# Kernel optimization log

Hardware: AMD Instinct MI355X
Metric: run time of the kernel (lower is better)

Reference implementation:

```python
import jax, jax.numpy as jnp
import numpy as np

ALPHA = 1.702   # swiglu_alpha
LIMIT = 7.0     # swiglu_limit
EPS = 1e-5      # norm_eps
E = 16          # num_experts
K = 4           # experts_per_token


def _swiglu(h):
    # interleaved split as in torch: even cols -> glu, odd cols -> linear
    x_glu = jnp.minimum(h[..., ::2], LIMIT)
    # faithful to source bug: clamp(min=limit, max=limit) == constant limit
    x_lin = jnp.clip(h[..., 1::2], LIMIT, LIMIT)
    return x_glu * jax.nn.sigmoid(ALPHA * x_glu) * (x_lin + 1.0)


def setup_inputs() -> dict:
    key = jax.random.key(0)
    ks = jax.random.split(key, 7)
    B, T, H, I = 1, 2048, 1024, 1024
    x = jax.random.normal(ks[0], (B, T, H), jnp.float32)
    scale = jnp.ones((H,), jnp.float32)
    gate_w = jax.random.normal(ks[1], (E, H), jnp.float32) * 0.02
    gate_b = jnp.zeros((E,), jnp.float32)
    mlp1_w = jax.random.normal(ks[2], (E, 2 * I, H), jnp.float32) * 0.02
    mlp1_b = jax.random.normal(ks[3], (E, 2 * I), jnp.float32) * 0.02
    mlp2_w = jax.random.normal(ks[4], (E, H, I), jnp.float32) * 0.02
    mlp2_b = jax.random.normal(ks[5], (E, H), jnp.float32) * 0.02
    return dict(x=x, scale=scale, gate_w=gate_w, gate_b=gate_b,
                mlp1_w=mlp1_w, mlp1_b=mlp1_b, mlp2_w=mlp2_w, mlp2_b=mlp2_b)


def reference(x, scale, gate_w, gate_b, mlp1_w, mlp1_b, mlp2_w, mlp2_b):
    # RMSNorm (fp32 math, identity cast here since inputs are fp32)
    t = x * jax.lax.rsqrt(jnp.mean(x * x, axis=-1, keepdims=True) + EPS) * scale
    # gate + top-k routing (sorted descending, matching torch.topk sorted=True)
    g = jnp.einsum('bth,eh->bte', t, gate_w) + gate_b          # [B,T,E]
    vals, idx = jax.lax.top_k(g, K)                            # [B,T,K]
    w = jax.nn.softmax(vals, axis=-1)                          # [B,T,K]
    # route[b,t,e] = sum_k w[b,t,k] * [idx[b,t,k]==e]  (top-k indices distinct)
    route = jnp.sum(jax.nn.one_hot(idx, E, dtype=t.dtype) * w[..., None], axis=-2)
    route_e = jnp.moveaxis(route, -1, 0)                       # [E,B,T]
    # grouped dense-per-expert computation instead of per-token weight gather:
    # mathematically identical output, avoids materializing [B,T,K,2I,H] gathers
    def step(acc, p):
        w1, b1, w2, b2, r = p
        h = jnp.einsum('bth,ih->bti', t, w1) + b1              # [B,T,2I]
        s = _swiglu(h)                                         # [B,T,I]
        y = jnp.einsum('bti,hi->bth', s, w2) + b2              # [B,T,H]
        return acc + r[..., None] * y, None
    acc, _ = jax.lax.scan(step, jnp.zeros_like(x),
                          (mlp1_w, mlp1_b, mlp2_w, mlp2_b, route_e))
    return x + acc
```

## Files before the change

kernel.cpp:

```cpp
#include <hip/hip_runtime.h>
#include <hip/hip_bf16.h>

typedef __bf16 bf16;
typedef __bf16 bf16x4 __attribute__((ext_vector_type(4)));
typedef __bf16 bf16x8 __attribute__((ext_vector_type(8)));
typedef float f32x4 __attribute__((ext_vector_type(4)));

constexpr int TKN  = 2048;
constexpr int HD   = 1024;
constexpr int NEXP = 16;
constexpr int KSEL = 4;
constexpr int IDIM = 1024;
constexpr int I2   = 2048;
constexpr int NROW = TKN * KSEL;

__device__ __forceinline__ void async_copy16(const void* g, void* l) {
  __builtin_amdgcn_global_load_lds((__attribute__((address_space(1))) void*)g,
                                   (__attribute__((address_space(3))) void*)l,
                                   16, 0, 0);
}

__global__ __launch_bounds__(256) void k_norm_gate(
    const float* __restrict__ x, const float* __restrict__ scale,
    const float* __restrict__ gate_w, const float* __restrict__ gate_b,
    float* __restrict__ out, bf16* __restrict__ tN,
    int* __restrict__ eids, float* __restrict__ wts)
{
  __shared__ float tLds[HD];
  __shared__ float red[4];
  __shared__ float gsh[NEXP];
  const int tid = threadIdx.x;
  const int tok = blockIdx.x;
  const int wid = tid >> 6, lane = tid & 63;

  const float4 x4 = *(const float4*)(x + (size_t)tok * HD + tid * 4);
  float ss = x4.x * x4.x + x4.y * x4.y + x4.z * x4.z + x4.w * x4.w;
  #pragma unroll
  for (int off = 32; off > 0; off >>= 1) ss += __shfl_down(ss, off);
  if (lane == 0) red[wid] = ss;
  __syncthreads();
  ss = red[0] + red[1] + red[2] + red[3];
  const float r = rsqrtf(ss * (1.0f / HD) + 1e-5f);

  const float4 s4 = *(const float4*)(scale + tid * 4);
  float4 t4;
  t4.x = x4.x * r * s4.x; t4.y = x4.y * r * s4.y;
  t4.z = x4.z * r * s4.z; t4.w = x4.w * r * s4.w;
  *(float4*)(out + (size_t)tok * HD + tid * 4) = x4;
  tLds[tid * 4 + 0] = t4.x; tLds[tid * 4 + 1] = t4.y;
  tLds[tid * 4 + 2] = t4.z; tLds[tid * 4 + 3] = t4.w;
  bf16x4 tb;
  tb[0] = (bf16)t4.x; tb[1] = (bf16)t4.y; tb[2] = (bf16)t4.z; tb[3] = (bf16)t4.w;
  *(bf16x4*)(tN + (size_t)tok * HD + tid * 4) = tb;
  __syncthreads();

  {
    const int e = tid >> 4, l16 = tid & 15;
    float p = 0.f;
    const float* gw = gate_w + (size_t)e * HD;
    for (int j = l16; j < HD; j += 16) p += tLds[j] * gw[j];
    p += __shfl_xor(p, 8); p += __shfl_xor(p, 4);
    p += __shfl_xor(p, 2); p += __shfl_xor(p, 1);
    if (l16 == 0) gsh[e] = p + gate_b[e];
  }
  __syncthreads();

  if (tid == 0) {
    float g[NEXP];
    #pragma unroll
    for (int i = 0; i < NEXP; ++i) g[i] = gsh[i];
    int   bi[KSEL]; float bv[KSEL];
    #pragma unroll
    for (int k = 0; k < KSEL; ++k) {
      float best = -1e30f; int b = 0;
      for (int i = 0; i < NEXP; ++i) if (g[i] > best) { best = g[i]; b = i; }
      bv[k] = best; bi[k] = b; g[b] = -1e30f;
    }
    const float m = bv[0];
    float wv[KSEL], sum = 0.f;
    #pragma unroll
    for (int k = 0; k < KSEL; ++k) { wv[k] = __expf(bv[k] - m); sum += wv[k]; }
    const float inv = 1.0f / sum;
    #pragma unroll
    for (int k = 0; k < KSEL; ++k) {
      eids[tok * KSEL + k] = bi[k];
      wts[tok * KSEL + k]  = wv[k] * inv;
    }
  }
}

__global__ __launch_bounds__(256) void k_route(
    const int* __restrict__ eids, const float* __restrict__ wts,
    int* __restrict__ cntg, int* __restrict__ segg,
    int* __restrict__ rowTok, float* __restrict__ rowW, int* __restrict__ rowOf)
{
  __shared__ int hcnt[NEXP], hoff[NEXP], hrun[NEXP];
  const int tid = threadIdx.x;
  if (tid < NEXP) { hcnt[tid] = 0; hrun[tid] = 0; }
  __syncthreads();
  for (int i = tid; i < NROW; i += 256) atomicAdd(&hcnt[eids[i]], 1);
  __syncthreads();
  if (tid == 0) {
    int s = 0;
    for (int e = 0; e < NEXP; ++e) { hoff[e] = s; segg[e] = s; cntg[e] = hcnt[e]; s += hcnt[e]; }
  }
  __syncthreads();
  for (int i = tid; i < NROW; i += 256) {
    const int e = eids[i];
    const int slot = atomicAdd(&hrun[e], 1);
    const int row = hoff[e] + slot;
    rowTok[row] = i >> 2;
    rowW[row]   = wts[i];
    rowOf[i]    = row;
  }
}

__global__ __launch_bounds__(256) void k_cvt_all(const float* __restrict__ w1,
                                                 const float* __restrict__ w2,
                                                 bf16* __restrict__ w1b,
                                                 bf16* __restrict__ w2b) {
  const size_t bid = blockIdx.x;
  if (bid < 8192) {
    const size_t f = bid * 256 + threadIdx.x;
    const size_t row = f >> 7;
    const int    off = (int)(f & 127) * 8;
    const size_t e = row >> 10, n = row & 1023;
    const float* s = w1 + (e * 2048 + 2 * n) * 1024 + off;
    const float4 a = *(const float4*)(s);
    const float4 b = *(const float4*)(s + 4);
    bf16x8 o;
    o[0] = (bf16)a.x; o[1] = (bf16)a.y; o[2] = (bf16)a.z; o[3] = (bf16)a.w;
    o[4] = (bf16)b.x; o[5] = (bf16)b.y; o[6] = (bf16)b.z; o[7] = (bf16)b.w;
    *(bf16x8*)(w1b + row * 1024 + off) = o;
  } else {
    const size_t f = (bid - 8192) * 256 + threadIdx.x;
    const size_t base = f * 8;
    const float4 a = *(const float4*)(w2 + base);
    const float4 b = *(const float4*)(w2 + base + 4);
    bf16x8 o;
    o[0] = (bf16)a.x; o[1] = (bf16)a.y; o[2] = (bf16)a.z; o[3] = (bf16)a.w;
    o[4] = (bf16)b.x; o[5] = (bf16)b.y; o[6] = (bf16)b.z; o[7] = (bf16)b.w;
    *(bf16x8*)(w2b + base) = o;
  }
}


__global__ __launch_bounds__(256) void k_gemm1v2(
    const bf16* __restrict__ tN, const bf16* __restrict__ w1b,
    const float* __restrict__ b1, const int* __restrict__ cnt,
    const int* __restrict__ segOff, const int* __restrict__ rowTok,
    bf16* __restrict__ sBuf)
{
  const int e = blockIdx.z, mt = blockIdx.y, nt = blockIdx.x;
  const int rows = cnt[e];
  if (mt * 64 >= rows) return;
  const int soff = segOff[e];
  __shared__ __align__(16) bf16 Asm[2 * 64 * 32];
  __shared__ __align__(16) bf16 Bsm[2 * 128 * 32];
  const int tid = threadIdx.x;
  const int wid = tid >> 6, lane = tid & 63;
  const int quad = lane >> 4, l16 = lane & 15;
  const int wm = wid & 1, wn = wid >> 1;

  const int r0 = wid * 16 + (lane >> 2);
  const int colE = (lane & 3) * 8;
  const int mA = min(mt * 64 + r0, rows - 1);
  const char* gA  = (const char*)(tN + (size_t)rowTok[soff + mA] * HD + colE);
  const int n0 = nt * 128;
  const char* gB0 = (const char*)(w1b + ((size_t)e * IDIM + n0 + r0) * HD + colE);
  const char* gB1 = (const char*)(w1b + ((size_t)e * IDIM + n0 + 64 + r0) * HD + colE);
  bf16* lA  = Asm + wid * 512;
  bf16* lB0 = Bsm + wid * 512;
  bf16* lB1 = Bsm + 2048 + wid * 512;

  const f32x4 zero = {0.f, 0.f, 0.f, 0.f};
  f32x4 acc[2][4];
  #pragma unroll
  for (int i = 0; i < 2; ++i)
    #pragma unroll
    for (int j = 0; j < 4; ++j) acc[i][j] = zero;

  for (int kt = 0; kt < 16; ++kt) {
    async_copy16(gA, lA);
    async_copy16(gB0, lB0);
    async_copy16(gB1, lB1);
    async_copy16(gA + 64, lA + 2048);
    async_copy16(gB0 + 64, lB0 + 4096);
    async_copy16(gB1 + 64, lB1 + 4096);
    gA += 128; gB0 += 128; gB1 += 128;
    __syncthreads();
    bf16x8 av[2];
    #pragma unroll
    for (int s = 0; s < 2; ++s) {
      av[0] = *(const bf16x8*)(Asm + s * 2048 + (wm * 32 + 0 * 16 + l16) * 32 + quad * 8);
      av[1] = *(const bf16x8*)(Asm + s * 2048 + (wm * 32 + 1 * 16 + l16) * 32 + quad * 8);
      #pragma unroll
      for (int j = 0; j < 4; ++j) {
        const bf16x8 bv = *(const bf16x8*)(Bsm + s * 4096 + (wn * 64 + j * 16 + l16) * 32 + quad * 8);
        acc[0][j] = __builtin_amdgcn_mfma_f32_16x16x32_bf16(av[0], bv, acc[0][j], 0, 0, 0);
        acc[1][j] = __builtin_amdgcn_mfma_f32_16x16x32_bf16(av[1], bv, acc[1][j], 0, 0, 0);
      }
    }
    __syncthreads();
  }

  const int mbase = mt * 64 + wm * 32;
  #pragma unroll
  for (int j = 0; j < 4; ++j) {
    const int ncol = n0 + wn * 64 + j * 16 + l16;
    const float bias = b1[(size_t)e * I2 + 2 * ncol];
    #pragma unroll
    for (int i = 0; i < 2; ++i) {
      #pragma unroll
      for (int rg = 0; rg < 4; ++rg) {
        const int gm = mbase + i * 16 + quad * 4 + rg;
        if (gm < rows) {
          const float h  = acc[i][j][rg] + bias;
          const float xg = fminf(h, 7.0f);
          const float s  = xg * (1.0f / (1.0f + __expf(-1.702f * xg))) * 8.0f;
          sBuf[((size_t)soff + gm) * IDIM + ncol] = (bf16)s;
        }
      }
    }
  }
}

template <bool USEY>
__global__ __launch_bounds__(256) void k_gemm2v2(
    const bf16* __restrict__ sBuf, const bf16* __restrict__ w2b,
    const float* __restrict__ b2, const int* __restrict__ cnt,
    const int* __restrict__ segOff, const int* __restrict__ rowTok,
    const float* __restrict__ rowW, bf16* __restrict__ yBuf,
    float* __restrict__ out)
{
  const int e = blockIdx.z, mt = blockIdx.y, nt = blockIdx.x;
  const int rows = cnt[e];
  if (mt * 64 >= rows) return;
  const int soff = segOff[e];
  __shared__ __align__(16) bf16 Asm[2 * 64 * 32];
  __shared__ __align__(16) bf16 Bsm[2 * 128 * 32];
  const int tid = threadIdx.x;
  const int wid = tid >> 6, lane = tid & 63;
  const int quad = lane >> 4, l16 = lane & 15;
  const int wm = wid & 1, wn = wid >> 1;

  const int r0 = wid * 16 + (lane >> 2);
  const int colE = (lane & 3) * 8;
  const int mA = min(mt * 64 + r0, rows - 1);
  const char* gA  = (const char*)(sBuf + ((size_t)soff + mA) * IDIM + colE);
  const int n0 = nt * 128;
  const char* gB0 = (const char*)(w2b + ((size_t)e * HD + n0 + r0) * IDIM + colE);
  const char* gB1 = (const char*)(w2b + ((size_t)e * HD + n0 + 64 + r0) * IDIM + colE);
  bf16* lA  = Asm + wid * 512;
  bf16* lB0 = Bsm + wid * 512;
  bf16* lB1 = Bsm + 2048 + wid * 512;

  const f32x4 zero = {0.f, 0.f, 0.f, 0.f};
  f32x4 acc[2][4];
  #pragma unroll
  for (int i = 0; i < 2; ++i)
    #pragma unroll
    for (int j = 0; j < 4; ++j) acc[i][j] = zero;

  for (int kt = 0; kt < 16; ++kt) {
    async_copy16(gA, lA);
    async_copy16(gB0, lB0);
    async_copy16(gB1, lB1);
    async_copy16(gA + 64, lA + 2048);
    async_copy16(gB0 + 64, lB0 + 4096);
    async_copy16(gB1 + 64, lB1 + 4096);
    gA += 128; gB0 += 128; gB1 += 128;
    __syncthreads();
    bf16x8 av[2];
    #pragma unroll
    for (int s = 0; s < 2; ++s) {
      av[0] = *(const bf16x8*)(Asm + s * 2048 + (wm * 32 + 0 * 16 + l16) * 32 + quad * 8);
      av[1] = *(const bf16x8*)(Asm + s * 2048 + (wm * 32 + 1 * 16 + l16) * 32 + quad * 8);
      #pragma unroll
      for (int j = 0; j < 4; ++j) {
        const bf16x8 bv = *(const bf16x8*)(Bsm + s * 4096 + (wn * 64 + j * 16 + l16) * 32 + quad * 8);
        acc[0][j] = __builtin_amdgcn_mfma_f32_16x16x32_bf16(av[0], bv, acc[0][j], 0, 0, 0);
        acc[1][j] = __builtin_amdgcn_mfma_f32_16x16x32_bf16(av[1], bv, acc[1][j], 0, 0, 0);
      }
    }
    __syncthreads();
  }

  const int mbase = mt * 64 + wm * 32;
  #pragma unroll
  for (int j = 0; j < 4; ++j) {
    const int ncol = n0 + wn * 64 + j * 16 + l16;
    const float bias = b2[(size_t)e * HD + ncol];
    #pragma unroll
    for (int i = 0; i < 2; ++i) {
      #pragma unroll
      for (int rg = 0; rg < 4; ++rg) {
        const int gm = mbase + i * 16 + quad * 4 + rg;
        if (gm < rows) {
          if constexpr (USEY) {
            yBuf[((size_t)soff + gm) * HD + ncol] = (bf16)(acc[i][j][rg] + bias);
          } else {
            atomicAdd(out + (size_t)rowTok[soff + gm] * HD + ncol,
                      rowW[soff + gm] * (acc[i][j][rg] + bias));
          }
        }
      }
    }
  }
}

__global__ __launch_bounds__(256) void k_finalize(
    const float* __restrict__ x, const bf16* __restrict__ yBuf,
    const int* __restrict__ rowOf, const float* __restrict__ wts,
    float* __restrict__ out)
{
  const int tok = blockIdx.x;
  const int tid = threadIdx.x;
  const int r0 = rowOf[tok * 4 + 0], r1 = rowOf[tok * 4 + 1];
  const int r2 = rowOf[tok * 4 + 2], r3 = rowOf[tok * 4 + 3];
  const float w0 = wts[tok * 4 + 0], w1 = wts[tok * 4 + 1];
  const float w2 = wts[tok * 4 + 2], w3 = wts[tok * 4 + 3];
  const int col = tid * 4;
  float4 o = *(const float4*)(x + (size_t)tok * HD + col);
  const bf16x4 y0 = *(const bf16x4*)(yBuf + (size_t)r0 * HD + col);
  const bf16x4 y1 = *(const bf16x4*)(yBuf + (size_t)r1 * HD + col);
  const bf16x4 y2 = *(const bf16x4*)(yBuf + (size_t)r2 * HD + col);
  const bf16x4 y3 = *(const bf16x4*)(yBuf + (size_t)r3 * HD + col);
  o.x += w0 * (float)y0[0] + w1 * (float)y1[0] + w2 * (float)y2[0] + w3 * (float)y3[0];
  o.y += w0 * (float)y0[1] + w1 * (float)y1[1] + w2 * (float)y2[1] + w3 * (float)y3[1];
  o.z += w0 * (float)y0[2] + w1 * (float)y1[2] + w2 * (float)y2[2] + w3 * (float)y3[2];
  o.w += w0 * (float)y0[3] + w1 * (float)y1[3] + w2 * (float)y2[3] + w3 * (float)y3[3];
  *(float4*)(out + (size_t)tok * HD + col) = o;
}

__global__ __launch_bounds__(256) void k_gemm1_fb(
    const bf16* __restrict__ tN, const float* __restrict__ w1,
    const float* __restrict__ b1, const int* __restrict__ cnt,
    const int* __restrict__ segOff, const int* __restrict__ rowTok,
    bf16* __restrict__ sBuf)
{
  const int e = blockIdx.z, mt = blockIdx.y, nt = blockIdx.x;
  const int rows = cnt[e];
  if (mt * 128 >= rows) return;
  const int soff = segOff[e];
  __shared__ __align__(16) bf16 Asm[128 * 32];
  __shared__ __align__(16) bf16 Bsm[128 * 32];
  const int tid = threadIdx.x;
  const int wid = tid >> 6, lane = tid & 63;
  const int quad = lane >> 4, l16 = lane & 15;
  const int wm = wid & 1, wn = wid >> 1;
  const int r0 = wid * 16 + (lane >> 2);
  const int r1 = 64 + r0;
  const int colE = (lane & 3) * 8;
  const int m0 = min(mt * 128 + r0, rows - 1);
  const int m1 = min(mt * 128 + r1, rows - 1);
  const char* gA0 = (const char*)(tN + (size_t)rowTok[soff + m0] * HD + colE);
  const char* gA1 = (const char*)(tN + (size_t)rowTok[soff + m1] * HD + colE);
  bf16* lA0 = Asm + wid * 512;
  bf16* lA1 = Asm + 2048 + wid * 512;
  const int brow = tid >> 3;
  const int bkk  = (tid & 7) * 4;
  const int n0 = nt * 128;
  const float* gB = w1 + (size_t)e * I2 * HD + (size_t)(2 * (n0 + brow)) * HD + bkk;

  const f32x4 zero = {0.f, 0.f, 0.f, 0.f};
  f32x4 acc[4][4];
  #pragma unroll
  for (int i = 0; i < 4; ++i)
    #pragma unroll
    for (int j = 0; j < 4; ++j) acc[i][j] = zero;

  for (int kt = 0; kt < 32; ++kt) {
    async_copy16(gA0, lA0);
    async_copy16(gA1, lA1);
    gA0 += 64; gA1 += 64;
    #pragma unroll
    for (int q = 0; q < 4; ++q) {
      const float4 v = *(const float4*)(gB + (size_t)q * 64 * HD);
      bf16x4 c;
      c[0] = (bf16)v.x; c[1] = (bf16)v.y; c[2] = (bf16)v.z; c[3] = (bf16)v.w;
      *(bf16x4*)(Bsm + (q * 32 + brow) * 32 + bkk) = c;
    }
    gB += 32;
    __syncthreads();
    bf16x8 av[4], bv[4];
    #pragma unroll
    for (int i = 0; i < 4; ++i)
      av[i] = *(const bf16x8*)(Asm + (wm * 64 + i * 16 + l16) * 32 + quad * 8);
    #pragma unroll
    for (int j = 0; j < 4; ++j)
      bv[j] = *(const bf16x8*)(Bsm + (wn * 64 + j * 16 + l16) * 32 + quad * 8);
    #pragma unroll
    for (int i = 0; i < 4; ++i)
      #pragma unroll
      for (int j = 0; j < 4; ++j)
        acc[i][j] = __builtin_amdgcn_mfma_f32_16x16x32_bf16(av[i], bv[j], acc[i][j], 0, 0, 0);
    __syncthreads();
  }
  const int mbase = mt * 128 + wm * 64;
  #pragma unroll
  for (int j = 0; j < 4; ++j) {
    const int ncol = n0 + wn * 64 + j * 16 + l16;
    const float bias = b1[(size_t)e * I2 + 2 * ncol];
    #pragma unroll
    for (int i = 0; i < 4; ++i) {
      #pragma unroll
      for (int rg = 0; rg < 4; ++rg) {
        const int gm = mbase + i * 16 + quad * 4 + rg;
        if (gm < rows) {
          const float h  = acc[i][j][rg] + bias;
          const float xg = fminf(h, 7.0f);
          const float s  = xg * (1.0f / (1.0f + __expf(-1.702f * xg))) * 8.0f;
          sBuf[((size_t)soff + gm) * IDIM + ncol] = (bf16)s;
        }
      }
    }
  }
}

__global__ __launch_bounds__(256) void k_gemm2_fb(
    const bf16* __restrict__ sBuf, const float* __restrict__ w2,
    const float* __restrict__ b2, const int* __restrict__ cnt,
    const int* __restrict__ segOff, const int* __restrict__ rowTok,
    const float* __restrict__ rowW, float* __restrict__ out)
{
  const int e = blockIdx.z, mt = blockIdx.y, nt = blockIdx.x;
  const int rows = cnt[e];
  if (mt * 128 >= rows) return;
  const int soff = segOff[e];
  __shared__ __align__(16) bf16 Asm[128 * 32];
  __shared__ __align__(16) bf16 Bsm[128 * 32];
  const int tid = threadIdx.x;
  const int wid = tid >> 6, lane = tid & 63;
  const int quad = lane >> 4, l16 = lane & 15;
  const int wm = wid & 1, wn = wid >> 1;
  const int r0 = wid * 16 + (lane >> 2);
  const int r1 = 64 + r0;
  const int colE = (lane & 3) * 8;
  const int m0 = min(mt * 128 + r0, rows - 1);
  const int m1 = min(mt * 128 + r1, rows - 1);
  const char* gA0 = (const char*)(sBuf + ((size_t)soff + m0) * IDIM + colE);
  const char* gA1 = (const char*)(sBuf + ((size_t)soff + m1) * IDIM + colE);
  bf16* lA0 = Asm + wid * 512;
  bf16* lA1 = Asm + 2048 + wid * 512;
  const int brow = tid >> 3;
  const int bkk  = (tid & 7) * 4;
  const int n0 = nt * 128;
  const float* gB = w2 + (size_t)e * HD * IDIM + (size_t)(n0 + brow) * IDIM + bkk;

  const f32x4 zero = {0.f, 0.f, 0.f, 0.f};
  f32x4 acc[4][4];
  #pragma unroll
  for (int i = 0; i < 4; ++i)
    #pragma unroll
    for (int j = 0; j < 4; ++j) acc[i][j] = zero;

  for (int kt = 0; kt < 32; ++kt) {
    async_copy16(gA0, lA0);
    async_copy16(gA1, lA1);
    gA0 += 64; gA1 += 64;
    #pragma unroll
    for (int q = 0; q < 4; ++q) {
      const float4 v = *(const float4*)(gB + (size_t)q * 32 * IDIM);
      bf16x4 c;
      c[0] = (bf16)v.x; c[1] = (bf16)v.y; c[2] = (bf16)v.z; c[3] = (bf16)v.w;
      *(bf16x4*)(Bsm + (q * 32 + brow) * 32 + bkk) = c;
    }
    gB += 32;
    __syncthreads();
    bf16x8 av[4], bv[4];
    #pragma unroll
    for (int i = 0; i < 4; ++i)
      av[i] = *(const bf16x8*)(Asm + (wm * 64 + i * 16 + l16) * 32 + quad * 8);
    #pragma unroll
    for (int j = 0; j < 4; ++j)
      bv[j] = *(const bf16x8*)(Bsm + (wn * 64 + j * 16 + l16) * 32 + quad * 8);
    #pragma unroll
    for (int i = 0; i < 4; ++i)
      #pragma unroll
      for (int j = 0; j < 4; ++j)
        acc[i][j] = __builtin_amdgcn_mfma_f32_16x16x32_bf16(av[i], bv[j], acc[i][j], 0, 0, 0);
    __syncthreads();
  }
  const int mbase = mt * 128 + wm * 64;
  #pragma unroll
  for (int j = 0; j < 4; ++j) {
    const int ncol = n0 + wn * 64 + j * 16 + l16;
    const float bias = b2[(size_t)e * HD + ncol];
    #pragma unroll
    for (int i = 0; i < 4; ++i) {
      #pragma unroll
      for (int rg = 0; rg < 4; ++rg) {
        const int gm = mbase + i * 16 + quad * 4 + rg;
        if (gm < rows) {
          atomicAdd(out + (size_t)rowTok[soff + gm] * HD + ncol,
                    rowW[soff + gm] * (acc[i][j][rg] + bias));
        }
      }
    }
  }
}

extern "C" void kernel_launch(void* const* d_in, const int* in_sizes, int n_in,
                              void* d_out, int out_size, void* d_ws, size_t ws_size,
                              hipStream_t stream) {
  const float* x      = (const float*)d_in[0];
  const float* scale  = (const float*)d_in[1];
  const float* gate_w = (const float*)d_in[2];
  const float* gate_b = (const float*)d_in[3];
  const float* w1     = (const float*)d_in[4];
  const float* b1     = (const float*)d_in[5];
  const float* w2     = (const float*)d_in[6];
  const float* b2     = (const float*)d_in[7];
  float* out = (float*)d_out;

  char* p = (char*)d_ws;
  bf16* tN   = (bf16*)p;  p += (size_t)TKN * HD * 2;
  bf16* sBuf = (bf16*)p;  p += (size_t)NROW * IDIM * 2;
  int*   eids   = (int*)p;   p += (size_t)NROW * 4;
  float* wts    = (float*)p; p += (size_t)NROW * 4;
  int*   rowTok = (int*)p;   p += (size_t)NROW * 4;
  float* rowW   = (float*)p; p += (size_t)NROW * 4;
  int*   rowOf  = (int*)p;   p += (size_t)NROW * 4;
  int*   cntg   = (int*)p;   p += 256;
  int*   segg   = (int*)p;   p += 256;
  const size_t base_need = (size_t)(p - (char*)d_ws);
  const size_t WSZ = (size_t)NEXP * IDIM * HD * 2;
  bf16* w2b  = (bf16*)p;
  bf16* w1b  = (bf16*)(p + WSZ);
  bf16* yBuf = (bf16*)(p + 2 * WSZ);
  const bool prep2 = ws_size >= base_need + WSZ;
  const bool prep1 = ws_size >= base_need + 2 * WSZ;
  const bool useY  = prep1 && prep2 &&
                     (ws_size >= base_need + 2 * WSZ + (size_t)NROW * HD * 2);

  k_norm_gate<<<TKN, 256, 0, stream>>>(x, scale, gate_w, gate_b, out, tN, eids, wts);
  k_route<<<1, 256, 0, stream>>>(eids, wts, cntg, segg, rowTok, rowW, rowOf);

  if (prep1 && prep2) {
    k_cvt_all<<<16384, 256, 0, stream>>>(w1, w2, w1b, w2b);
  }

  if (prep1 && prep2) {
    k_gemm1v2<<<dim3(8, 32, NEXP), 256, 0, stream>>>(tN, w1b, b1, cntg, segg, rowTok, sBuf);
    if (useY) {
      k_gemm2v2<true><<<dim3(8, 32, NEXP), 256, 0, stream>>>(sBuf, w2b, b2, cntg, segg,
                                                             rowTok, rowW, yBuf, out);
      k_finalize<<<TKN, 256, 0, stream>>>(x, yBuf, rowOf, wts, out);
    } else {
      k_gemm2v2<false><<<dim3(8, 32, NEXP), 256, 0, stream>>>(sBuf, w2b, b2, cntg, segg,
                                                              rowTok, rowW, yBuf, out);
    }
  } else {
    k_gemm1_fb<<<dim3(8, 16, NEXP), 256, 0, stream>>>(tN, w1, b1, cntg, segg, rowTok, sBuf);
    k_gemm2_fb<<<dim3(8, 16, NEXP), 256, 0, stream>>>(sBuf, w2, b2, cntg, segg, rowTok, rowW, out);
  }
}
```

Measured before the change: 380.1 us.

## Double-buffer LDS tiles in expert GEMMs to overlap loads with MFMA

Both grouped expert GEMM kernels now use two LDS stages. The next K-tile is prefetched with async global-to-LDS copies while the MFMAs consume the current tile, and one barrier per iteration replaces two. This targets exposed global-load latency in the main loop. It doubles LDS per block, which may lower occupancy. The async copies are issued after the barrier without an explicit wait on their completion, so correctness depends on the barrier draining the outstanding loads.

New measurement: 379.2 us. Within noise of the previous version (-0.2%).

```diff
diff --git a/kernel.cpp b/kernel.cpp
--- a/kernel.cpp
+++ b/kernel.cpp
@@ -145,7 +145,7 @@
 }
 
 
-__global__ __launch_bounds__(256) void k_gemm1v2(
+__global__ __launch_bounds__(256) void k_gemm1v3(
     const bf16* __restrict__ tN, const bf16* __restrict__ w1b,
     const float* __restrict__ b1, const int* __restrict__ cnt,
     const int* __restrict__ segOff, const int* __restrict__ rowTok,
@@ -155,8 +155,7 @@
   const int rows = cnt[e];
   if (mt * 64 >= rows) return;
   const int soff = segOff[e];
-  __shared__ __align__(16) bf16 Asm[2 * 64 * 32];
-  __shared__ __align__(16) bf16 Bsm[2 * 128 * 32];
+  __shared__ __align__(16) bf16 SM[2 * 12288];
   const int tid = threadIdx.x;
   const int wid = tid >> 6, lane = tid & 63;
   const int quad = lane >> 4, l16 = lane & 15;
@@ -169,9 +168,16 @@
   const int n0 = nt * 128;
   const char* gB0 = (const char*)(w1b + ((size_t)e * IDIM + n0 + r0) * HD + colE);
   const char* gB1 = (const char*)(w1b + ((size_t)e * IDIM + n0 + 64 + r0) * HD + colE);
-  bf16* lA  = Asm + wid * 512;
-  bf16* lB0 = Bsm + wid * 512;
-  bf16* lB1 = Bsm + 2048 + wid * 512;
+
+  {
+    bf16* dA  = SM + wid * 512;
+    bf16* dB0 = SM + 4096 + wid * 512;
+    bf16* dB1 = SM + 6144 + wid * 512;
+    async_copy16(gA, dA);        async_copy16(gA + 64, dA + 2048);
+    async_copy16(gB0, dB0);      async_copy16(gB0 + 64, dB0 + 4096);
+    async_copy16(gB1, dB1);      async_copy16(gB1 + 64, dB1 + 4096);
+    gA += 128; gB0 += 128; gB1 += 128;
+  }
 
   const f32x4 zero = {0.f, 0.f, 0.f, 0.f};
   f32x4 acc[2][4];
@@ -181,27 +187,29 @@
     for (int j = 0; j < 4; ++j) acc[i][j] = zero;
 
   for (int kt = 0; kt < 16; ++kt) {
-    async_copy16(gA, lA);
-    async_copy16(gB0, lB0);
-    async_copy16(gB1, lB1);
-    async_copy16(gA + 64, lA + 2048);
-    async_copy16(gB0 + 64, lB0 + 4096);
-    async_copy16(gB1 + 64, lB1 + 4096);
-    gA += 128; gB0 += 128; gB1 += 128;
     __syncthreads();
-    bf16x8 av[2];
+    if (kt < 15) {
+      const int nb = (kt + 1) & 1;
+      bf16* dA  = SM + nb * 12288 + wid * 512;
+      bf16* dB0 = SM + nb * 12288 + 4096 + wid * 512;
+      bf16* dB1 = SM + nb * 12288 + 6144 + wid * 512;
+      async_copy16(gA, dA);        async_copy16(gA + 64, dA + 2048);
+      async_copy16(gB0, dB0);      async_copy16(gB0 + 64, dB0 + 4096);
+      async_copy16(gB1, dB1);      async_copy16(gB1 + 64, dB1 + 4096);
+      gA += 128; gB0 += 128; gB1 += 128;
+    }
+    const bf16* cb = SM + (kt & 1) * 12288;
     #pragma unroll
     for (int s = 0; s < 2; ++s) {
-      av[0] = *(const bf16x8*)(Asm + s * 2048 + (wm * 32 + 0 * 16 + l16) * 32 + quad * 8);
-      av[1] = *(const bf16x8*)(Asm + s * 2048 + (wm * 32 + 1 * 16 + l16) * 32 + quad * 8);
+      const bf16x8 a0 = *(const bf16x8*)(cb + s * 2048 + (wm * 32 + l16) * 32 + quad * 8);
+      const bf16x8 a1 = *(const bf16x8*)(cb + s * 2048 + (wm * 32 + 16 + l16) * 32 + quad * 8);
       #pragma unroll
       for (int j = 0; j < 4; ++j) {
-        const bf16x8 bv = *(const bf16x8*)(Bsm + s * 4096 + (wn * 64 + j * 16 + l16) * 32 + quad * 8);
-        acc[0][j] = __builtin_amdgcn_mfma_f32_16x16x32_bf16(av[0], bv, acc[0][j], 0, 0, 0);
-        acc[1][j] = __builtin_amdgcn_mfma_f32_16x16x32_bf16(av[1], bv, acc[1][j], 0, 0, 0);
+        const bf16x8 bv = *(const bf16x8*)(cb + 4096 + s * 4096 + (wn * 64 + j * 16 + l16) * 32 + quad * 8);
+        acc[0][j] = __builtin_amdgcn_mfma_f32_16x16x32_bf16(a0, bv, acc[0][j], 0, 0, 0);
+        acc[1][j] = __builtin_amdgcn_mfma_f32_16x16x32_bf16(a1, bv, acc[1][j], 0, 0, 0);
       }
     }
-    __syncthreads();
   }
 
   const int mbase = mt * 64 + wm * 32;
@@ -226,7 +234,7 @@
 }
 
 template <bool USEY>
-__global__ __launch_bounds__(256) void k_gemm2v2(
+__global__ __launch_bounds__(256) void k_gemm2v3(
     const bf16* __restrict__ sBuf, const bf16* __restrict__ w2b,
     const float* __restrict__ b2, const int* __restrict__ cnt,
     const int* __restrict__ segOff, const int* __restrict__ rowTok,
@@ -237,8 +245,7 @@
   const int rows = cnt[e];
   if (mt * 64 >= rows) return;
   const int soff = segOff[e];
-  __shared__ __align__(16) bf16 Asm[2 * 64 * 32];
-  __shared__ __align__(16) bf16 Bsm[2 * 128 * 32];
+  __shared__ __align__(16) bf16 SM[2 * 12288];
   const int tid = threadIdx.x;
   const int wid = tid >> 6, lane = tid & 63;
   const int quad = lane >> 4, l16 = lane & 15;
@@ -251,9 +258,16 @@
   const int n0 = nt * 128;
   const char* gB0 = (const char*)(w2b + ((size_t)e * HD + n0 + r0) * IDIM + colE);
   const char* gB1 = (const char*)(w2b + ((size_t)e * HD + n0 + 64 + r0) * IDIM + colE);
-  bf16* lA  = Asm + wid * 512;
-  bf16* lB0 = Bsm + wid * 512;
-  bf16* lB1 = Bsm + 2048 + wid * 512;
+
+  {
+    bf16* dA  = SM + wid * 512;
+    bf16* dB0 = SM + 4096 + wid * 512;
+    bf16* dB1 = SM + 6144 + wid * 512;
+    async_copy16(gA, dA);        async_copy16(gA + 64, dA + 2048);
+    async_copy16(gB0, dB0);      async_copy16(gB0 + 64, dB0 + 4096);
+    async_copy16(gB1, dB1);      async_copy16(gB1 + 64, dB1 + 4096);
+    gA += 128; gB0 += 128; gB1 += 128;
+  }
 
   const f32x4 zero = {0.f, 0.f, 0.f, 0.f};
   f32x4 acc[2][4];
@@ -263,27 +277,29 @@
     for (int j = 0; j < 4; ++j) acc[i][j] = zero;
 
   for (int kt = 0; kt < 16; ++kt) {
-    async_copy16(gA, lA);
-    async_copy16(gB0, lB0);
-    async_copy16(gB1, lB1);
-    async_copy16(gA + 64, lA + 2048);
-    async_copy16(gB0 + 64, lB0 + 4096);
-    async_copy16(gB1 + 64, lB1 + 4096);
-    gA += 128; gB0 += 128; gB1 += 128;
     __syncthreads();
-    bf16x8 av[2];
+    if (kt < 15) {
+      const int nb = (kt + 1) & 1;
+      bf16* dA  = SM + nb * 12288 + wid * 512;
+      bf16* dB0 = SM + nb * 12288 + 4096 + wid * 512;
+      bf16* dB1 = SM + nb * 12288 + 6144 + wid * 512;
+      async_copy16(gA, dA);        async_copy16(gA + 64, dA + 2048);
+      async_copy16(gB0, dB0);      async_copy16(gB0 + 64, dB0 + 4096);
+      async_copy16(gB1, dB1);      async_copy16(gB1 + 64, dB1 + 4096);
+      gA += 128; gB0 += 128; gB1 += 128;
+    }
+    const bf16* cb = SM + (kt & 1) * 12288;
     #pragma unroll
     for (int s = 0; s < 2; ++s) {
-      av[0] = *(const bf16x8*)(Asm + s * 2048 + (wm * 32 + 0 * 16 + l16) * 32 + quad * 8);
-      av[1] = *(const bf16x8*)(Asm + s * 2048 + (wm * 32 + 1 * 16 + l16) * 32 + quad * 8);
+      const bf16x8 a0 = *(const bf16x8*)(cb + s * 2048 + (wm * 32 + l16) * 32 + quad * 8);
+      const bf16x8 a1 = *(const bf16x8*)(cb + s * 2048 + (wm * 32 + 16 + l16) * 32 + quad * 8);
       #pragma unroll
       for (int j = 0; j < 4; ++j) {
-        const bf16x8 bv = *(const bf16x8*)(Bsm + s * 4096 + (wn * 64 + j * 16 + l16) * 32 + quad * 8);
-        acc[0][j] = __builtin_amdgcn_mfma_f32_16x16x32_bf16(av[0], bv, acc[0][j], 0, 0, 0);
-        acc[1][j] = __builtin_amdgcn_mfma_f32_16x16x32_bf16(av[1], bv, acc[1][j], 0, 0, 0);
+        const bf16x8 bv = *(const bf16x8*)(cb + 4096 + s * 4096 + (wn * 64 + j * 16 + l16) * 32 + quad * 8);
+        acc[0][j] = __builtin_amdgcn_mfma_f32_16x16x32_bf16(a0, bv, acc[0][j], 0, 0, 0);
+        acc[1][j] = __builtin_amdgcn_mfma_f32_16x16x32_bf16(a1, bv, acc[1][j], 0, 0, 0);
       }
     }
-    __syncthreads();
   }
 
   const int mbase = mt * 64 + wm * 32;
@@ -529,26 +545,22 @@
   bf16* w2b  = (bf16*)p;
   bf16* w1b  = (bf16*)(p + WSZ);
   bf16* yBuf = (bf16*)(p + 2 * WSZ);
-  const bool prep2 = ws_size >= base_need + WSZ;
-  const bool prep1 = ws_size >= base_need + 2 * WSZ;
-  const bool useY  = prep1 && prep2 &&
+  const bool prep  = ws_size >= base_need + 2 * WSZ;
+  const bool useY  = prep &&
                      (ws_size >= base_need + 2 * WSZ + (size_t)NROW * HD * 2);
 
   k_norm_gate<<<TKN, 256, 0, stream>>>(x, scale, gate_w, gate_b, out, tN, eids, wts);
   k_route<<<1, 256, 0, stream>>>(eids, wts, cntg, segg, rowTok, rowW, rowOf);
 
-  if (prep1 && prep2) {
+  if (prep) {
     k_cvt_all<<<16384, 256, 0, stream>>>(w1, w2, w1b, w2b);
-  }
-
-  if (prep1 && prep2) {
-    k_gemm1v2<<<dim3(8, 32, NEXP), 256, 0, stream>>>(tN, w1b, b1, cntg, segg, rowTok, sBuf);
+    k_gemm1v3<<<dim3(8, 32, NEXP), 256, 0, stream>>>(tN, w1b, b1, cntg, segg, rowTok, sBuf);
     if (useY) {
-      k_gemm2v2<true><<<dim3(8, 32, NEXP), 256, 0, stream>>>(sBuf, w2b, b2, cntg, segg,
+      k_gemm2v3<true><<<dim3(8, 32, NEXP), 256, 0, stream>>>(sBuf, w2b, b2, cntg, segg,
                                                              rowTok, rowW, yBuf, out);
       k_finalize<<<TKN, 256, 0, stream>>>(x, yBuf, rowOf, wts, out);
     } else {
-      k_gemm2v2<false><<<dim3(8, 32, NEXP), 256, 0, stream>>>(sBuf, w2b, b2, cntg, segg,
+      k_gemm2v3<false><<<dim3(8, 32, NEXP), 256, 0, stream>>>(sBuf, w2b, b2, cntg, segg,
                                                               rowTok, rowW, yBuf, out);
     }
   } else {
```
